# Optimization experiments

Hardware: AMD Instinct MI355X
Metric: run time of the kernel (lower is better)

## Reference

```python
import jax, jax.numpy as jnp
import numpy as np
import math

B_ = 32      # input capsule types
C_ = 32      # output capsule types
K = 3        # kernel
STRIDE = 2
H = 4
HH = H * H
ITER = 3
EPS = 1e-10
LN_2PI = math.log(2.0 * math.pi)


def setup_inputs() -> dict:
    key = jax.random.key(0)
    k1, k2, k3, k4, k5 = jax.random.split(key, 5)
    b, win = 8, 14
    poses = jax.random.normal(k1, (b, B_, win, win, HH), jnp.float32)
    activations = jax.random.uniform(k2, (b, B_, win, win), jnp.float32)
    W = jax.random.normal(k3, (B_, K, K, C_, H, H), jnp.float32)
    beta_v = jax.random.normal(k4, (1, C_, 1, 1), jnp.float32)
    beta_a = jax.random.normal(k5, (1, C_, 1), jnp.float32)
    lambda_ = jnp.float32(0.01)
    return {"poses": poses, "activations": activations, "W": W,
            "beta_v": beta_v, "beta_a": beta_a, "lambda_": lambda_}


def _extract_patches(x, w):
    r = STRIDE * jnp.arange(w)[:, None] + jnp.arange(K)  # [w, K]
    x = x[:, :, r]
    x = x[:, :, :, :, r]        # index width   -> [b,B,w_i,Kr,w_j,Kc,...]
    return x


def _em_routing(lambda_, a_, V, beta_v, beta_a):
    # a_: [b,Bkk,Cww], V: [b,Bkk,Cww,hh]
    b, Bkk, Cww, hh = V.shape
    R = jnp.full((b, Bkk, Cww), 1.0 / C_, V.dtype)
    a = None
    mu = None
    for i in range(ITER):
        Rw = (R * a_)[..., None]                      # [b,Bkk,Cww,1]
        sum_R = Rw.sum(1)                             # [b,Cww,1]
        mu = ((Rw * V).sum(1) / sum_R)[:, None]       # [b,1,Cww,hh]
        V_minus_mu_sqr = (V - mu) ** 2                # [b,Bkk,Cww,hh]
        sigma_sq = ((Rw * V_minus_mu_sqr).sum(1) / sum_R)[:, None]  # [b,1,Cww,hh]
        log_sigma = jnp.log(jnp.sqrt(sigma_sq) + EPS)
        cost = (beta_v + log_sigma.reshape(b, C_, -1, hh)) * sum_R.reshape(b, C_, -1, 1)
        a = jax.nn.sigmoid(lambda_ * (beta_a - cost.sum(-1)))
        a = a.reshape(b, Cww)
        if i != ITER - 1:
            ln_p = -V_minus_mu_sqr / (2.0 * sigma_sq) - log_sigma - 0.5 * LN_2PI
            p = jnp.exp(ln_p)
            ap = a[:, None, :] * p.sum(-1)            # [b,Bkk,Cww]
            R = jax.lax.stop_gradient(ap / (ap.sum(2, keepdims=True) + EPS) + EPS)
    return a, mu


def reference(poses, activations, W, beta_v, beta_a, lambda_):
    b = poses.shape[0]
    win = poses.shape[2]
    w = (win - K) // STRIDE + 1
    Bkk = K * K * B_
    Cww = w * w * C_

    # pose patches, ordered exactly like torch: stacked over (j outer, i inner)
    pp = _extract_patches(poses, w)                 # [b,B,w_i,Kr,w_j,Kc,hh]
    pp = pp.transpose(0, 1, 3, 5, 4, 2, 6)          # [b,B,Kr,Kc,w_j,w_i,hh]
    pp = pp.reshape(b, B_, K, K, w, w, H, H)

    # votes: W[B,Kr,Kc,C,p,q] @ pose[...,q,r]
    votes = jnp.einsum('Buvcpq,bBuvxyqr->bBuvcxypr', W, pp)
    votes = votes.reshape(b, Bkk, Cww, HH)

    # activation patches, repeated over C to match Cww=(C,w,w) flatten order
    ap = _extract_patches(activations, w)           # [b,B,w_i,Kr,w_j,Kc]
    ap = ap.transpose(0, 1, 3, 5, 4, 2).reshape(b, Bkk, w * w)
    a_ = jnp.broadcast_to(ap[:, :, None, :], (b, Bkk, C_, w * w)).reshape(b, Bkk, Cww)

    a, mu = _em_routing(lambda_, a_, votes, beta_v, beta_a)
    return mu.reshape(b, C_, w, w, HH), a.reshape(b, C_, w, w)
```

## Files before the change

### kernel.cpp

```cpp
#include <hip/hip_runtime.h>
#include <math.h>

#define NB   8
#define BC   32
#define WIN  14
#define HH   16
#define BKK  288
#define CWW  1152
#define NXY  36
#define EPSF 1e-10f
#define LOG2E 1.4426950408889634f
#define LN2   0.6931471805599453f
#define L2SQ2PI 1.3257480647361593f

__device__ __forceinline__ float ex2(float x) { return __builtin_amdgcn_exp2f(x); }
__device__ __forceinline__ float lg2(float x) { return __builtin_amdgcn_logf(x); }
__device__ __forceinline__ float rcpf(float x) { return __builtin_amdgcn_rcpf(x); }

__device__ __forceinline__ float red16(float v) {
    v += __shfl_xor(v, 1);
    v += __shfl_xor(v, 2);
    v += __shfl_xor(v, 4);
    v += __shfl_xor(v, 8);
    return v;
}

__device__ __forceinline__ float4 f4mul(float s, float4 b) {
    return make_float4(s * b.x, s * b.y, s * b.z, s * b.w);
}
__device__ __forceinline__ float4 f4fma(float s, float4 b, float4 c) {
    return make_float4(fmaf(s, b.x, c.x), fmaf(s, b.y, c.y),
                       fmaf(s, b.z, c.z), fmaf(s, b.w, c.w));
}

__global__ __launch_bounds__(256)
void wt_kernel(const float4* __restrict__ W4, float4* __restrict__ Wt4) {
    int o = blockIdx.x * 256 + threadIdx.x;
    if (o < BKK * 128) {
        int c = o & 31, p = (o >> 5) & 3, m = o >> 7;
        Wt4[o] = W4[(m * 32 + c) * 4 + p];
    }
}

__global__ __launch_bounds__(256)
void rowred_kernel(const float* __restrict__ rows_part, float* __restrict__ invRowG) {
    int i = blockIdx.x * 256 + threadIdx.x;
    if (i < NB * BKK) {
        int b = i / BKK, m = i % BKK;
        float s = EPSF;
        #pragma unroll 8
        for (int j = 0; j < 72; ++j) s += rows_part[(b * 72 + j) * BKK + m];
        invRowG[i] = 1.0f / s;
    }
}

template<int STAGE, bool FINAL>
__global__ __launch_bounds__(256)
void stats_kernel(const float* __restrict__ poses,
                  const float* __restrict__ act,
                  const float4* __restrict__ Wt4,
                  const float* __restrict__ beta_v,
                  const float* __restrict__ beta_a,
                  const float* __restrict__ lam,
                  const float* __restrict__ aws_in,
                  const float* __restrict__ psum,
                  const float* __restrict__ invRowG,
                  float* __restrict__ mu_out,
                  float* __restrict__ K2n_out,
                  float* __restrict__ C2n_out,
                  float* __restrict__ a_out)
{
    __shared__ float4 poseS4[BKK * 4];
    __shared__ float2 AE[BKK];
    __shared__ float4 red4[4 * 16 * 9];

    const int bid   = blockIdx.x;
    const int chalf = bid & 1;
    const int xy    = (bid >> 1) % NXY;
    const int b     = bid / 72;
    const int X = xy / 6, Y = xy % 6;

    const int tid = threadIdx.x;
    const int c_l = tid & 15;
    const int mch = tid >> 4;
    const int c   = chalf * 16 + c_l;
    const int n   = c * NXY + xy;

    const float4* poses4 = reinterpret_cast<const float4*>(poses);
    for (int idx = tid; idx < BKK * 4; idx += 256) {
        int m = idx >> 2, q = idx & 3;
        int B = m / 9, uv = m % 9, u = uv / 3, v = uv % 3;
        poseS4[idx] = poses4[((b * BC + B) * 196 + (2 * Y + u) * WIN + (2 * X + v)) * 4 + q];
    }
    for (int m = tid; m < BKK; m += 256) {
        int B = m / 9, uv = m % 9, u = uv / 3, v = uv % 3;
        float am = act[(b * BC + B) * 196 + (2 * Y + u) * WIN + (2 * X + v)];
        float ai, ea;
        if constexpr (STAGE == 0) { ai = am * (1.0f / 32.0f); ea = 0.0f; }
        else { ai = am * invRowG[b * BKK + m]; ea = EPSF * am; }
        AE[m] = make_float2(ai, ea);
    }

    float ap_n = 0.0f;
    const float* psum_b = nullptr;
    if constexpr (STAGE >= 1) {
        ap_n   = aws_in[(b * NXY + xy) * 32 + c];
        psum_b = psum + ((b * BKK) * NXY + xy) * 32 + c;
    }
    __syncthreads();

    const float4* WtB = Wt4 + c;

    float  sum_R = 0.0f;
    float4 sRV[4]  = {make_float4(0,0,0,0), make_float4(0,0,0,0), make_float4(0,0,0,0), make_float4(0,0,0,0)};
    float4 sRV2[4] = {make_float4(0,0,0,0), make_float4(0,0,0,0), make_float4(0,0,0,0), make_float4(0,0,0,0)};

    const int m0 = mch * 18;
    #pragma unroll 3
    for (int i = 0; i < 18; ++i) {
        int m = m0 + i;
        float4 w0 = WtB[m * 128 +  0];
        float4 w1 = WtB[m * 128 + 32];
        float4 w2 = WtB[m * 128 + 64];
        float4 w3 = WtB[m * 128 + 96];
        float4 P0 = poseS4[m * 4 + 0];
        float4 P1 = poseS4[m * 4 + 1];
        float4 P2 = poseS4[m * 4 + 2];
        float4 P3 = poseS4[m * 4 + 3];
        float4 V0 = f4fma(w0.w, P3, f4fma(w0.z, P2, f4fma(w0.y, P1, f4mul(w0.x, P0))));
        float4 V1 = f4fma(w1.w, P3, f4fma(w1.z, P2, f4fma(w1.y, P1, f4mul(w1.x, P0))));
        float4 V2 = f4fma(w2.w, P3, f4fma(w2.z, P2, f4fma(w2.y, P1, f4mul(w2.x, P0))));
        float4 V3 = f4fma(w3.w, P3, f4fma(w3.z, P2, f4fma(w3.y, P1, f4mul(w3.x, P0))));
        float Ra;
        if constexpr (STAGE == 0) {
            Ra = AE[m].x;
        } else {
            float ps = psum_b[m * (NXY * 32)];
            float2 ae = AE[m];
            Ra = fmaf(ap_n * ps, ae.x, ae.y);
        }
        sum_R += Ra;
        sRV[0] = f4fma(Ra, V0, sRV[0]);
        sRV[1] = f4fma(Ra, V1, sRV[1]);
        sRV[2] = f4fma(Ra, V2, sRV[2]);
        sRV[3] = f4fma(Ra, V3, sRV[3]);
        float4 q0 = make_float4(V0.x*V0.x, V0.y*V0.y, V0.z*V0.z, V0.w*V0.w);
        float4 q1 = make_float4(V1.x*V1.x, V1.y*V1.y, V1.z*V1.z, V1.w*V1.w);
        float4 q2 = make_float4(V2.x*V2.x, V2.y*V2.y, V2.z*V2.z, V2.w*V2.w);
        float4 q3 = make_float4(V3.x*V3.x, V3.y*V3.y, V3.z*V3.z, V3.w*V3.w);
        sRV2[0] = f4fma(Ra, q0, sRV2[0]);
        sRV2[1] = f4fma(Ra, q1, sRV2[1]);
        sRV2[2] = f4fma(Ra, q2, sRV2[2]);
        sRV2[3] = f4fma(Ra, q3, sRV2[3]);
    }

    {
        float* f1 = reinterpret_cast<float*>(sRV);
        float* f2 = reinterpret_cast<float*>(sRV2);
        #pragma unroll
        for (int k = 0; k < 16; ++k) { f1[k] += __shfl_xor(f1[k], 16); f2[k] += __shfl_xor(f2[k], 16); }
        sum_R += __shfl_xor(sum_R, 16);
        #pragma unroll
        for (int k = 0; k < 16; ++k) { f1[k] += __shfl_xor(f1[k], 32); f2[k] += __shfl_xor(f2[k], 32); }
        sum_R += __shfl_xor(sum_R, 32);
    }
    const int wgrp = tid >> 6;
    if ((tid & 48) == 0) {
        float4* dst = &red4[(wgrp * 16 + c_l) * 9];
        dst[0] = make_float4(sum_R, 0.f, 0.f, 0.f);
        dst[1] = sRV[0];  dst[2] = sRV[1];  dst[3] = sRV[2];  dst[4] = sRV[3];
        dst[5] = sRV2[0]; dst[6] = sRV2[1]; dst[7] = sRV2[2]; dst[8] = sRV2[3];
    }
    __syncthreads();

    const int h  = tid & 15;
    const int cc = tid >> 4;
    const float* red = reinterpret_cast<const float*>(red4);
    float sR = 0.f, sV = 0.f, sV2 = 0.f;
    #pragma unroll
    for (int j = 0; j < 4; ++j) {
        int off = (j * 16 + cc) * 36;
        sR  += red[off];
        sV  += red[off + 4 + h];
        sV2 += red[off + 20 + h];
    }
    float inv = 1.0f / sR;
    float mu  = sV * inv;
    float sig = fmaxf(fmaf(-mu, mu, sV2 * inv), 1e-30f);
    float l2s = lg2(sqrtf(sig) + EPSF);
    float lsum = red16(l2s) * LN2;
    int   cg   = chalf * 16 + cc;
    float cost = sR * fmaf(16.0f, beta_v[cg], lsum);
    float z    = lam[0] * (beta_a[cg] - cost);
    float av   = rcpf(1.0f + ex2(-z * LOG2E));

    int nn   = cg * NXY + xy;
    int base = (b * CWW + nn) * HH + h;
    mu_out[base] = mu;
    if constexpr (!FINAL) {
        K2n_out[base] = (-0.5f * LOG2E) / sig;
        C2n_out[base] = -(l2s + L2SQ2PI);
        if (h == 0) a_out[(b * NXY + xy) * 32 + cg] = av;
    } else {
        if (h == 0) a_out[b * CWW + nn] = av;
    }
}

__global__ __launch_bounds__(256)
void pv_kernel(const float* __restrict__ poses,
               const float4* __restrict__ Wt4,
               const float4* __restrict__ mu4,
               const float4* __restrict__ K4,
               const float4* __restrict__ C4,
               const float* __restrict__ aws,
               float* __restrict__ psum_out,
               float* __restrict__ rows_part)
{
    __shared__ float4 poseS4[BKK * 4];

    const int bid   = blockIdx.x;
    const int chalf = bid & 1;
    const int xy    = (bid >> 1) % NXY;
    const int b     = bid / 72;
    const int X = xy / 6, Y = xy % 6;

    const int tid = threadIdx.x;
    const int c_l = tid & 15;
    const int mch = tid >> 4;
    const int c   = chalf * 16 + c_l;
    const int n   = c * NXY + xy;

    const float4* poses4 = reinterpret_cast<const float4*>(poses);
    for (int idx = tid; idx < BKK * 4; idx += 256) {
        int m = idx >> 2, q = idx & 3;
        int B = m / 9, uv = m % 9, u = uv / 3, v = uv % 3;
        poseS4[idx] = poses4[((b * BC + B) * 196 + (2 * Y + u) * WIN + (2 * X + v)) * 4 + q];
    }

    float4 M[4], Kk[4], Cc[4];
    {
        int nb4 = (b * CWW + n) * 4;
        #pragma unroll
        for (int p = 0; p < 4; ++p) { M[p] = mu4[nb4 + p]; Kk[p] = K4[nb4 + p]; Cc[p] = C4[nb4 + p]; }
    }
    const float ap = aws[(b * NXY + xy) * 32 + c];
    __syncthreads();

    const float4* WtB = Wt4 + c;
    float* ps_out = psum_out + ((b * BKK) * NXY + xy) * 32 + c;
    const int rbase = bid * BKK;

    const int m0 = mch * 18;
    #pragma unroll 3
    for (int i = 0; i < 18; ++i) {
        int m = m0 + i;
        float4 w0 = WtB[m * 128 +  0];
        float4 w1 = WtB[m * 128 + 32];
        float4 w2 = WtB[m * 128 + 64];
        float4 w3 = WtB[m * 128 + 96];
        float4 P0 = poseS4[m * 4 + 0];
        float4 P1 = poseS4[m * 4 + 1];
        float4 P2 = poseS4[m * 4 + 2];
        float4 P3 = poseS4[m * 4 + 3];
        float4 V0 = f4fma(w0.w, P3, f4fma(w0.z, P2, f4fma(w0.y, P1, f4mul(w0.x, P0))));
        float4 V1 = f4fma(w1.w, P3, f4fma(w1.z, P2, f4fma(w1.y, P1, f4mul(w1.x, P0))));
        float4 V2 = f4fma(w2.w, P3, f4fma(w2.z, P2, f4fma(w2.y, P1, f4mul(w2.x, P0))));
        float4 V3 = f4fma(w3.w, P3, f4fma(w3.z, P2, f4fma(w3.y, P1, f4mul(w3.x, P0))));

        float psv = 0.0f;
        {
            float4 t, g;
            t = make_float4(V0.x-M[0].x, V0.y-M[0].y, V0.z-M[0].z, V0.w-M[0].w);
            g = make_float4(fmaf(t.x*t.x, Kk[0].x, Cc[0].x), fmaf(t.y*t.y, Kk[0].y, Cc[0].y),
                            fmaf(t.z*t.z, Kk[0].z, Cc[0].z), fmaf(t.w*t.w, Kk[0].w, Cc[0].w));
            psv += ex2(g.x) + ex2(g.y) + ex2(g.z) + ex2(g.w);
            t = make_float4(V1.x-M[1].x, V1.y-M[1].y, V1.z-M[1].z, V1.w-M[1].w);
            g = make_float4(fmaf(t.x*t.x, Kk[1].x, Cc[1].x), fmaf(t.y*t.y, Kk[1].y, Cc[1].y),
                            fmaf(t.z*t.z, Kk[1].z, Cc[1].z), fmaf(t.w*t.w, Kk[1].w, Cc[1].w));
            psv += ex2(g.x) + ex2(g.y) + ex2(g.z) + ex2(g.w);
            t = make_float4(V2.x-M[2].x, V2.y-M[2].y, V2.z-M[2].z, V2.w-M[2].w);
            g = make_float4(fmaf(t.x*t.x, Kk[2].x, Cc[2].x), fmaf(t.y*t.y, Kk[2].y, Cc[2].y),
                            fmaf(t.z*t.z, Kk[2].z, Cc[2].z), fmaf(t.w*t.w, Kk[2].w, Cc[2].w));
            psv += ex2(g.x) + ex2(g.y) + ex2(g.z) + ex2(g.w);
            t = make_float4(V3.x-M[3].x, V3.y-M[3].y, V3.z-M[3].z, V3.w-M[3].w);
            g = make_float4(fmaf(t.x*t.x, Kk[3].x, Cc[3].x), fmaf(t.y*t.y, Kk[3].y, Cc[3].y),
                            fmaf(t.z*t.z, Kk[3].z, Cc[3].z), fmaf(t.w*t.w, Kk[3].w, Cc[3].w));
            psv += ex2(g.x) + ex2(g.y) + ex2(g.z) + ex2(g.w);
        }
        ps_out[m * (NXY * 32)] = psv;

        float rv = ap * psv;
        rv += __shfl_xor(rv, 1);
        rv += __shfl_xor(rv, 2);
        rv += __shfl_xor(rv, 4);
        rv += __shfl_xor(rv, 8);
        if (c_l == 0) rows_part[rbase + m] = rv;
    }
}

extern "C" void kernel_launch(void* const* d_in, const int* in_sizes, int n_in,
                              void* d_out, int out_size, void* d_ws, size_t ws_size,
                              hipStream_t stream) {
    const float* poses  = (const float*)d_in[0];
    const float* act    = (const float*)d_in[1];
    const float* W      = (const float*)d_in[2];
    const float* beta_v = (const float*)d_in[3];
    const float* beta_a = (const float*)d_in[4];
    const float* lam    = (const float*)d_in[5];
    float* out = (float*)d_out;
    float* ws  = (float*)d_ws;

    const int SZ = NB * CWW * HH;
    float* Wt   = ws;
    float* mu   = Wt + SZ;
    float* K2n  = mu + SZ;
    float* C2n  = K2n + SZ;
    float* aws  = C2n + SZ;
    float* rows = aws + NB * CWW;
    float* invR = rows + NB * 72 * BKK;
    float* psum = invR + NB * BKK;

    const float4* Wt4 = (const float4*)Wt;

    wt_kernel<<<dim3(144), dim3(256), 0, stream>>>((const float4*)W, (float4*)Wt);

    stats_kernel<0, false><<<dim3(576), dim3(256), 0, stream>>>(
        poses, act, Wt4, beta_v, beta_a, lam, nullptr, nullptr, nullptr,
        mu, K2n, C2n, aws);
    pv_kernel<<<dim3(576), dim3(256), 0, stream>>>(
        poses, Wt4, (const float4*)mu, (const float4*)K2n, (const float4*)C2n,
        aws, psum, rows);
    rowred_kernel<<<dim3(9), dim3(256), 0, stream>>>(rows, invR);
    stats_kernel<1, false><<<dim3(576), dim3(256), 0, stream>>>(
        poses, act, Wt4, beta_v, beta_a, lam, aws, psum, invR,
        mu, K2n, C2n, aws);
    pv_kernel<<<dim3(576), dim3(256), 0, stream>>>(
        poses, Wt4, (const float4*)mu, (const float4*)K2n, (const float4*)C2n,
        aws, psum, rows);
    rowred_kernel<<<dim3(9), dim3(256), 0, stream>>>(rows, invR);
    stats_kernel<1, true><<<dim3(576), dim3(256), 0, stream>>>(
        poses, act, Wt4, beta_v, beta_a, lam, aws, psum, invR,
        out, nullptr, nullptr, out + SZ);
}
```

Before: 179.8 us.

## Fuse EM routing iterations into one persistent kernel with grid barriers

Replaces the chain of stats, pv and row-reduction kernels with a single persistent kernel. Each block keeps its pose tile, per-capsule mu, K and C terms and the p-sums in shared memory across iterations. Blocks sync through a software grid barrier built on atomics, and each block then computes the row normalisation redundantly for its batch. This removes several launches and the global round-trips of mu, K, C and psum, but it relies on all 576 blocks being co-resident (launch_bounds 256,3) and adds barrier spin cost.

```diff
diff --git a/kernel.cpp b/kernel.cpp
--- a/kernel.cpp
+++ b/kernel.cpp
@@ -8,6 +8,7 @@
 #define BKK  288
 #define CWW  1152
 #define NXY  36
+#define NBLK 576
 #define EPSF 1e-10f
 #define LOG2E 1.4426950408889634f
 #define LN2   0.6931471805599453f
@@ -33,46 +34,58 @@
                        fmaf(s, b.z, c.z), fmaf(s, b.w, c.w));
 }
 
+__device__ __forceinline__ void grid_barrier(unsigned* cnt, unsigned* gen) {
+    __threadfence();
+    __syncthreads();
+    if (threadIdx.x == 0) {
+        unsigned g = __hip_atomic_load(gen, __ATOMIC_RELAXED, __HIP_MEMORY_SCOPE_AGENT);
+        unsigned prev = __hip_atomic_fetch_add(cnt, 1u, __ATOMIC_ACQ_REL, __HIP_MEMORY_SCOPE_AGENT);
+        if (prev == NBLK - 1u) {
+            __hip_atomic_store(cnt, 0u, __ATOMIC_RELAXED, __HIP_MEMORY_SCOPE_AGENT);
+            __threadfence();
+            __hip_atomic_fetch_add(gen, 1u, __ATOMIC_RELEASE, __HIP_MEMORY_SCOPE_AGENT);
+        } else {
+            while (__hip_atomic_load(gen, __ATOMIC_RELAXED, __HIP_MEMORY_SCOPE_AGENT) == g) {
+                __builtin_amdgcn_s_sleep(2);
+            }
+        }
+    }
+    __syncthreads();
+    __threadfence();
+}
+
 __global__ __launch_bounds__(256)
-void wt_kernel(const float4* __restrict__ W4, float4* __restrict__ Wt4) {
+void wt_kernel(const float4* __restrict__ W4, float4* __restrict__ Wt4,
+               unsigned* __restrict__ bar) {
     int o = blockIdx.x * 256 + threadIdx.x;
+    if (o < 2) bar[o] = 0u;
     if (o < BKK * 128) {
         int c = o & 31, p = (o >> 5) & 3, m = o >> 7;
         Wt4[o] = W4[(m * 32 + c) * 4 + p];
     }
 }
 
-__global__ __launch_bounds__(256)
-void rowred_kernel(const float* __restrict__ rows_part, float* __restrict__ invRowG) {
-    int i = blockIdx.x * 256 + threadIdx.x;
-    if (i < NB * BKK) {
-        int b = i / BKK, m = i % BKK;
-        float s = EPSF;
-        #pragma unroll 8
-        for (int j = 0; j < 72; ++j) s += rows_part[(b * 72 + j) * BKK + m];
-        invRowG[i] = 1.0f / s;
-    }
-}
-
-template<int STAGE, bool FINAL>
-__global__ __launch_bounds__(256)
-void stats_kernel(const float* __restrict__ poses,
-                  const float* __restrict__ act,
-                  const float4* __restrict__ Wt4,
-                  const float* __restrict__ beta_v,
-                  const float* __restrict__ beta_a,
-                  const float* __restrict__ lam,
-                  const float* __restrict__ aws_in,
-                  const float* __restrict__ psum,
-                  const float* __restrict__ invRowG,
-                  float* __restrict__ mu_out,
-                  float* __restrict__ K2n_out,
-                  float* __restrict__ C2n_out,
-                  float* __restrict__ a_out)
+__global__ __launch_bounds__(256, 3)
+void fused_em(const float* __restrict__ poses,
+              const float* __restrict__ act,
+              const float4* __restrict__ Wt4,
+              const float* __restrict__ beta_v,
+              const float* __restrict__ beta_a,
+              const float* __restrict__ lam,
+              float* __restrict__ rows0,
+              float* __restrict__ rows1,
+              unsigned* __restrict__ bar,
+              float* __restrict__ mu_out,
+              float* __restrict__ a_out)
 {
     __shared__ float4 poseS4[BKK * 4];
+    __shared__ float  amL[BKK];
     __shared__ float2 AE[BKK];
-    __shared__ float4 red4[4 * 16 * 9];
+    __shared__ float  muL[16][17];
+    __shared__ float  KL[16][17];
+    __shared__ float  CL[16][17];
+    __shared__ float  aL[16];
+    __shared__ __align__(16) float uni[BKK * 17];
 
     const int bid   = blockIdx.x;
     const int chalf = bid & 1;
@@ -84,7 +97,7 @@
     const int c_l = tid & 15;
     const int mch = tid >> 4;
     const int c   = chalf * 16 + c_l;
-    const int n   = c * NXY + xy;
+    const int m0  = mch * 18;
 
     const float4* poses4 = reinterpret_cast<const float4*>(poses);
     for (int idx = tid; idx < BKK * 4; idx += 256) {
@@ -95,206 +108,182 @@
     for (int m = tid; m < BKK; m += 256) {
         int B = m / 9, uv = m % 9, u = uv / 3, v = uv % 3;
         float am = act[(b * BC + B) * 196 + (2 * Y + u) * WIN + (2 * X + v)];
-        float ai, ea;
-        if constexpr (STAGE == 0) { ai = am * (1.0f / 32.0f); ea = 0.0f; }
-        else { ai = am * invRowG[b * BKK + m]; ea = EPSF * am; }
-        AE[m] = make_float2(ai, ea);
-    }
-
-    float ap_n = 0.0f;
-    const float* psum_b = nullptr;
-    if constexpr (STAGE >= 1) {
-        ap_n   = aws_in[(b * NXY + xy) * 32 + c];
-        psum_b = psum + ((b * BKK) * NXY + xy) * 32 + c;
-    }
+        amL[m] = am;
+        AE[m] = make_float2(am * (1.0f / 32.0f), 0.0f);
+    }
+    for (int i = tid; i < BKK * 17; i += 256) uni[i] = 0.0f;
+    if (tid < 16) aL[tid] = 0.0f;
     __syncthreads();
 
-    const float4* WtB = Wt4 + c;
-
-    float  sum_R = 0.0f;
-    float4 sRV[4]  = {make_float4(0,0,0,0), make_float4(0,0,0,0), make_float4(0,0,0,0), make_float4(0,0,0,0)};
-    float4 sRV2[4] = {make_float4(0,0,0,0), make_float4(0,0,0,0), make_float4(0,0,0,0), make_float4(0,0,0,0)};
-
-    const int m0 = mch * 18;
-    #pragma unroll 3
-    for (int i = 0; i < 18; ++i) {
-        int m = m0 + i;
-        float4 w0 = WtB[m * 128 +  0];
-        float4 w1 = WtB[m * 128 + 32];
-        float4 w2 = WtB[m * 128 + 64];
-        float4 w3 = WtB[m * 128 + 96];
-        float4 P0 = poseS4[m * 4 + 0];
-        float4 P1 = poseS4[m * 4 + 1];
-        float4 P2 = poseS4[m * 4 + 2];
-        float4 P3 = poseS4[m * 4 + 3];
-        float4 V0 = f4fma(w0.w, P3, f4fma(w0.z, P2, f4fma(w0.y, P1, f4mul(w0.x, P0))));
-        float4 V1 = f4fma(w1.w, P3, f4fma(w1.z, P2, f4fma(w1.y, P1, f4mul(w1.x, P0))));
-        float4 V2 = f4fma(w2.w, P3, f4fma(w2.z, P2, f4fma(w2.y, P1, f4mul(w2.x, P0))));
-        float4 V3 = f4fma(w3.w, P3, f4fma(w3.z, P2, f4fma(w3.y, P1, f4mul(w3.x, P0))));
-        float Ra;
-        if constexpr (STAGE == 0) {
-            Ra = AE[m].x;
-        } else {
-            float ps = psum_b[m * (NXY * 32)];
+    const float4* WtB  = Wt4 + c;
+    const float   lamv = lam[0];
+    float4* red4 = reinterpret_cast<float4*>(uni);
+    unsigned* bcnt = bar;
+    unsigned* bgen = bar + 1;
+
+    for (int it = 0; it < 3; ++it) {
+        const float ap_n = aL[c_l];
+        float  sum_R = 0.0f;
+        float4 sRV[4]  = {make_float4(0,0,0,0), make_float4(0,0,0,0),
+                          make_float4(0,0,0,0), make_float4(0,0,0,0)};
+        float4 sRV2[4] = {make_float4(0,0,0,0), make_float4(0,0,0,0),
+                          make_float4(0,0,0,0), make_float4(0,0,0,0)};
+        #pragma unroll 3
+        for (int i = 0; i < 18; ++i) {
+            const int m = m0 + i;
+            float4 w0 = WtB[m * 128 +  0];
+            float4 w1 = WtB[m * 128 + 32];
+            float4 w2 = WtB[m * 128 + 64];
+            float4 w3 = WtB[m * 128 + 96];
+            float4 P0 = poseS4[m * 4 + 0];
+            float4 P1 = poseS4[m * 4 + 1];
+            float4 P2 = poseS4[m * 4 + 2];
+            float4 P3 = poseS4[m * 4 + 3];
+            float4 V0 = f4fma(w0.w, P3, f4fma(w0.z, P2, f4fma(w0.y, P1, f4mul(w0.x, P0))));
+            float4 V1 = f4fma(w1.w, P3, f4fma(w1.z, P2, f4fma(w1.y, P1, f4mul(w1.x, P0))));
+            float4 V2 = f4fma(w2.w, P3, f4fma(w2.z, P2, f4fma(w2.y, P1, f4mul(w2.x, P0))));
+            float4 V3 = f4fma(w3.w, P3, f4fma(w3.z, P2, f4fma(w3.y, P1, f4mul(w3.x, P0))));
             float2 ae = AE[m];
-            Ra = fmaf(ap_n * ps, ae.x, ae.y);
-        }
-        sum_R += Ra;
-        sRV[0] = f4fma(Ra, V0, sRV[0]);
-        sRV[1] = f4fma(Ra, V1, sRV[1]);
-        sRV[2] = f4fma(Ra, V2, sRV[2]);
-        sRV[3] = f4fma(Ra, V3, sRV[3]);
-        float4 q0 = make_float4(V0.x*V0.x, V0.y*V0.y, V0.z*V0.z, V0.w*V0.w);
-        float4 q1 = make_float4(V1.x*V1.x, V1.y*V1.y, V1.z*V1.z, V1.w*V1.w);
-        float4 q2 = make_float4(V2.x*V2.x, V2.y*V2.y, V2.z*V2.z, V2.w*V2.w);
-        float4 q3 = make_float4(V3.x*V3.x, V3.y*V3.y, V3.z*V3.z, V3.w*V3.w);
-        sRV2[0] = f4fma(Ra, q0, sRV2[0]);
-        sRV2[1] = f4fma(Ra, q1, sRV2[1]);
-        sRV2[2] = f4fma(Ra, q2, sRV2[2]);
-        sRV2[3] = f4fma(Ra, q3, sRV2[3]);
-    }
-
-    {
-        float* f1 = reinterpret_cast<float*>(sRV);
-        float* f2 = reinterpret_cast<float*>(sRV2);
+            float Ra;
+            if (it == 0) Ra = ae.x;
+            else         Ra = fmaf(ap_n * uni[m * 17 + c_l], ae.x, ae.y);
+            sum_R += Ra;
+            sRV[0] = f4fma(Ra, V0, sRV[0]);
+            sRV[1] = f4fma(Ra, V1, sRV[1]);
+            sRV[2] = f4fma(Ra, V2, sRV[2]);
+            sRV[3] = f4fma(Ra, V3, sRV[3]);
+            float4 q0 = make_float4(V0.x*V0.x, V0.y*V0.y, V0.z*V0.z, V0.w*V0.w);
+            float4 q1 = make_float4(V1.x*V1.x, V1.y*V1.y, V1.z*V1.z, V1.w*V1.w);
+            float4 q2 = make_float4(V2.x*V2.x, V2.y*V2.y, V2.z*V2.z, V2.w*V2.w);
+            float4 q3 = make_float4(V3.x*V3.x, V3.y*V3.y, V3.z*V3.z, V3.w*V3.w);
+            sRV2[0] = f4fma(Ra, q0, sRV2[0]);
+            sRV2[1] = f4fma(Ra, q1, sRV2[1]);
+            sRV2[2] = f4fma(Ra, q2, sRV2[2]);
+            sRV2[3] = f4fma(Ra, q3, sRV2[3]);
+        }
+
+        {
+            float* f1 = reinterpret_cast<float*>(sRV);
+            float* f2 = reinterpret_cast<float*>(sRV2);
+            #pragma unroll
+            for (int k = 0; k < 16; ++k) { f1[k] += __shfl_xor(f1[k], 16); f2[k] += __shfl_xor(f2[k], 16); }
+            sum_R += __shfl_xor(sum_R, 16);
+            #pragma unroll
+            for (int k = 0; k < 16; ++k) { f1[k] += __shfl_xor(f1[k], 32); f2[k] += __shfl_xor(f2[k], 32); }
+            sum_R += __shfl_xor(sum_R, 32);
+        }
+        __syncthreads();
+        if ((tid & 48) == 0) {
+            float4* dst = &red4[((tid >> 6) * 16 + c_l) * 9];
+            dst[0] = make_float4(sum_R, 0.f, 0.f, 0.f);
+            dst[1] = sRV[0];  dst[2] = sRV[1];  dst[3] = sRV[2];  dst[4] = sRV[3];
+            dst[5] = sRV2[0]; dst[6] = sRV2[1]; dst[7] = sRV2[2]; dst[8] = sRV2[3];
+        }
+        __syncthreads();
+
+        {
+            const int h  = tid & 15;
+            const int cc = tid >> 4;
+            float sR = 0.f, sV = 0.f, sV2 = 0.f;
+            #pragma unroll
+            for (int j = 0; j < 4; ++j) {
+                int off = (j * 16 + cc) * 36;
+                sR  += uni[off];
+                sV  += uni[off + 4 + h];
+                sV2 += uni[off + 20 + h];
+            }
+            float inv = 1.0f / sR;
+            float mu  = sV * inv;
+            float sig = fmaxf(fmaf(-mu, mu, sV2 * inv), 1e-30f);
+            float l2s = lg2(sqrtf(sig) + EPSF);
+            float lsum = red16(l2s) * LN2;
+            int   cgi  = chalf * 16 + cc;
+            float cost = sR * fmaf(16.0f, beta_v[cgi], lsum);
+            float z    = lamv * (beta_a[cgi] - cost);
+            float av   = rcpf(1.0f + ex2(-z * LOG2E));
+            if (it < 2) {
+                muL[cc][h] = mu;
+                KL[cc][h]  = (-0.5f * LOG2E) / sig;
+                CL[cc][h]  = -(l2s + L2SQ2PI);
+                if (h == 0) aL[cc] = av;
+            } else {
+                int nn   = cgi * NXY + xy;
+                int base = (b * CWW + nn) * HH + h;
+                mu_out[base] = mu;
+                if (h == 0) a_out[b * CWW + nn] = av;
+            }
+        }
+        if (it == 2) return;
+        __syncthreads();
+
+        float4 M[4], Kk[4], Cc[4];
         #pragma unroll
-        for (int k = 0; k < 16; ++k) { f1[k] += __shfl_xor(f1[k], 16); f2[k] += __shfl_xor(f2[k], 16); }
-        sum_R += __shfl_xor(sum_R, 16);
-        #pragma unroll
-        for (int k = 0; k < 16; ++k) { f1[k] += __shfl_xor(f1[k], 32); f2[k] += __shfl_xor(f2[k], 32); }
-        sum_R += __shfl_xor(sum_R, 32);
-    }
-    const int wgrp = tid >> 6;
-    if ((tid & 48) == 0) {
-        float4* dst = &red4[(wgrp * 16 + c_l) * 9];
-        dst[0] = make_float4(sum_R, 0.f, 0.f, 0.f);
-        dst[1] = sRV[0];  dst[2] = sRV[1];  dst[3] = sRV[2];  dst[4] = sRV[3];
-        dst[5] = sRV2[0]; dst[6] = sRV2[1]; dst[7] = sRV2[2]; dst[8] = sRV2[3];
-    }
-    __syncthreads();
-
-    const int h  = tid & 15;
-    const int cc = tid >> 4;
-    const float* red = reinterpret_cast<const float*>(red4);
-    float sR = 0.f, sV = 0.f, sV2 = 0.f;
-    #pragma unroll
-    for (int j = 0; j < 4; ++j) {
-        int off = (j * 16 + cc) * 36;
-        sR  += red[off];
-        sV  += red[off + 4 + h];
-        sV2 += red[off + 20 + h];
-    }
-    float inv = 1.0f / sR;
-    float mu  = sV * inv;
-    float sig = fmaxf(fmaf(-mu, mu, sV2 * inv), 1e-30f);
-    float l2s = lg2(sqrtf(sig) + EPSF);
-    float lsum = red16(l2s) * LN2;
-    int   cg   = chalf * 16 + cc;
-    float cost = sR * fmaf(16.0f, beta_v[cg], lsum);
-    float z    = lam[0] * (beta_a[cg] - cost);
-    float av   = rcpf(1.0f + ex2(-z * LOG2E));
-
-    int nn   = cg * NXY + xy;
-    int base = (b * CWW + nn) * HH + h;
-    mu_out[base] = mu;
-    if constexpr (!FINAL) {
-        K2n_out[base] = (-0.5f * LOG2E) / sig;
-        C2n_out[base] = -(l2s + L2SQ2PI);
-        if (h == 0) a_out[(b * NXY + xy) * 32 + cg] = av;
-    } else {
-        if (h == 0) a_out[b * CWW + nn] = av;
-    }
-}
-
-__global__ __launch_bounds__(256)
-void pv_kernel(const float* __restrict__ poses,
-               const float4* __restrict__ Wt4,
-               const float4* __restrict__ mu4,
-               const float4* __restrict__ K4,
-               const float4* __restrict__ C4,
-               const float* __restrict__ aws,
-               float* __restrict__ psum_out,
-               float* __restrict__ rows_part)
-{
-    __shared__ float4 poseS4[BKK * 4];
-
-    const int bid   = blockIdx.x;
-    const int chalf = bid & 1;
-    const int xy    = (bid >> 1) % NXY;
-    const int b     = bid / 72;
-    const int X = xy / 6, Y = xy % 6;
-
-    const int tid = threadIdx.x;
-    const int c_l = tid & 15;
-    const int mch = tid >> 4;
-    const int c   = chalf * 16 + c_l;
-    const int n   = c * NXY + xy;
-
-    const float4* poses4 = reinterpret_cast<const float4*>(poses);
-    for (int idx = tid; idx < BKK * 4; idx += 256) {
-        int m = idx >> 2, q = idx & 3;
-        int B = m / 9, uv = m % 9, u = uv / 3, v = uv % 3;
-        poseS4[idx] = poses4[((b * BC + B) * 196 + (2 * Y + u) * WIN + (2 * X + v)) * 4 + q];
-    }
-
-    float4 M[4], Kk[4], Cc[4];
-    {
-        int nb4 = (b * CWW + n) * 4;
-        #pragma unroll
-        for (int p = 0; p < 4; ++p) { M[p] = mu4[nb4 + p]; Kk[p] = K4[nb4 + p]; Cc[p] = C4[nb4 + p]; }
-    }
-    const float ap = aws[(b * NXY + xy) * 32 + c];
-    __syncthreads();
-
-    const float4* WtB = Wt4 + c;
-    float* ps_out = psum_out + ((b * BKK) * NXY + xy) * 32 + c;
-    const int rbase = bid * BKK;
-
-    const int m0 = mch * 18;
-    #pragma unroll 3
-    for (int i = 0; i < 18; ++i) {
-        int m = m0 + i;
-        float4 w0 = WtB[m * 128 +  0];
-        float4 w1 = WtB[m * 128 + 32];
-        float4 w2 = WtB[m * 128 + 64];
-        float4 w3 = WtB[m * 128 + 96];
-        float4 P0 = poseS4[m * 4 + 0];
-        float4 P1 = poseS4[m * 4 + 1];
-        float4 P2 = poseS4[m * 4 + 2];
-        float4 P3 = poseS4[m * 4 + 3];
-        float4 V0 = f4fma(w0.w, P3, f4fma(w0.z, P2, f4fma(w0.y, P1, f4mul(w0.x, P0))));
-        float4 V1 = f4fma(w1.w, P3, f4fma(w1.z, P2, f4fma(w1.y, P1, f4mul(w1.x, P0))));
-        float4 V2 = f4fma(w2.w, P3, f4fma(w2.z, P2, f4fma(w2.y, P1, f4mul(w2.x, P0))));
-        float4 V3 = f4fma(w3.w, P3, f4fma(w3.z, P2, f4fma(w3.y, P1, f4mul(w3.x, P0))));
-
-        float psv = 0.0f;
-        {
-            float4 t, g;
-            t = make_float4(V0.x-M[0].x, V0.y-M[0].y, V0.z-M[0].z, V0.w-M[0].w);
-            g = make_float4(fmaf(t.x*t.x, Kk[0].x, Cc[0].x), fmaf(t.y*t.y, Kk[0].y, Cc[0].y),
-                            fmaf(t.z*t.z, Kk[0].z, Cc[0].z), fmaf(t.w*t.w, Kk[0].w, Cc[0].w));
-            psv += ex2(g.x) + ex2(g.y) + ex2(g.z) + ex2(g.w);
-            t = make_float4(V1.x-M[1].x, V1.y-M[1].y, V1.z-M[1].z, V1.w-M[1].w);
-            g = make_float4(fmaf(t.x*t.x, Kk[1].x, Cc[1].x), fmaf(t.y*t.y, Kk[1].y, Cc[1].y),
-                            fmaf(t.z*t.z, Kk[1].z, Cc[1].z), fmaf(t.w*t.w, Kk[1].w, Cc[1].w));
-            psv += ex2(g.x) + ex2(g.y) + ex2(g.z) + ex2(g.w);
-            t = make_float4(V2.x-M[2].x, V2.y-M[2].y, V2.z-M[2].z, V2.w-M[2].w);
-            g = make_float4(fmaf(t.x*t.x, Kk[2].x, Cc[2].x), fmaf(t.y*t.y, Kk[2].y, Cc[2].y),
-                            fmaf(t.z*t.z, Kk[2].z, Cc[2].z), fmaf(t.w*t.w, Kk[2].w, Cc[2].w));
-            psv += ex2(g.x) + ex2(g.y) + ex2(g.z) + ex2(g.w);
-            t = make_float4(V3.x-M[3].x, V3.y-M[3].y, V3.z-M[3].z, V3.w-M[3].w);
-            g = make_float4(fmaf(t.x*t.x, Kk[3].x, Cc[3].x), fmaf(t.y*t.y, Kk[3].y, Cc[3].y),
-                            fmaf(t.z*t.z, Kk[3].z, Cc[3].z), fmaf(t.w*t.w, Kk[3].w, Cc[3].w));
-            psv += ex2(g.x) + ex2(g.y) + ex2(g.z) + ex2(g.w);
-        }
-        ps_out[m * (NXY * 32)] = psv;
-
-        float rv = ap * psv;
-        rv += __shfl_xor(rv, 1);
-        rv += __shfl_xor(rv, 2);
-        rv += __shfl_xor(rv, 4);
-        rv += __shfl_xor(rv, 8);
-        if (c_l == 0) rows_part[rbase + m] = rv;
+        for (int p = 0; p < 4; ++p) {
+            M[p]  = make_float4(muL[c_l][4*p+0], muL[c_l][4*p+1], muL[c_l][4*p+2], muL[c_l][4*p+3]);
+            Kk[p] = make_float4(KL[c_l][4*p+0],  KL[c_l][4*p+1],  KL[c_l][4*p+2],  KL[c_l][4*p+3]);
+            Cc[p] = make_float4(CL[c_l][4*p+0],  CL[c_l][4*p+1],  CL[c_l][4*p+2],  CL[c_l][4*p+3]);
+        }
+        const float ap = aL[c_l];
+        float* rowsW = (it == 0 ? rows0 : rows1) + bid * BKK;
+
+        #pragma unroll 3
+        for (int i = 0; i < 18; ++i) {
+            const int m = m0 + i;
+            float4 w0 = WtB[m * 128 +  0];
+            float4 w1 = WtB[m * 128 + 32];
+            float4 w2 = WtB[m * 128 + 64];
+            float4 w3 = WtB[m * 128 + 96];
+            float4 P0 = poseS4[m * 4 + 0];
+            float4 P1 = poseS4[m * 4 + 1];
+            float4 P2 = poseS4[m * 4 + 2];
+            float4 P3 = poseS4[m * 4 + 3];
+            float4 V0 = f4fma(w0.w, P3, f4fma(w0.z, P2, f4fma(w0.y, P1, f4mul(w0.x, P0))));
+            float4 V1 = f4fma(w1.w, P3, f4fma(w1.z, P2, f4fma(w1.y, P1, f4mul(w1.x, P0))));
+            float4 V2 = f4fma(w2.w, P3, f4fma(w2.z, P2, f4fma(w2.y, P1, f4mul(w2.x, P0))));
+            float4 V3 = f4fma(w3.w, P3, f4fma(w3.z, P2, f4fma(w3.y, P1, f4mul(w3.x, P0))));
+
+            float psv = 0.0f;
+            {
+                float4 t, g;
+                t = make_float4(V0.x-M[0].x, V0.y-M[0].y, V0.z-M[0].z, V0.w-M[0].w);
+                g = make_float4(fmaf(t.x*t.x, Kk[0].x, Cc[0].x), fmaf(t.y*t.y, Kk[0].y, Cc[0].y),
+                                fmaf(t.z*t.z, Kk[0].z, Cc[0].z), fmaf(t.w*t.w, Kk[0].w, Cc[0].w));
+                psv += ex2(g.x) + ex2(g.y) + ex2(g.z) + ex2(g.w);
+                t = make_float4(V1.x-M[1].x, V1.y-M[1].y, V1.z-M[1].z, V1.w-M[1].w);
+                g = make_float4(fmaf(t.x*t.x, Kk[1].x, Cc[1].x), fmaf(t.y*t.y, Kk[1].y, Cc[1].y),
+                                fmaf(t.z*t.z, Kk[1].z, Cc[1].z), fmaf(t.w*t.w, Kk[1].w, Cc[1].w));
+                psv += ex2(g.x) + ex2(g.y) + ex2(g.z) + ex2(g.w);
+                t = make_float4(V2.x-M[2].x, V2.y-M[2].y, V2.z-M[2].z, V2.w-M[2].w);
+                g = make_float4(fmaf(t.x*t.x, Kk[2].x, Cc[2].x), fmaf(t.y*t.y, Kk[2].y, Cc[2].y),
+                                fmaf(t.z*t.z, Kk[2].z, Cc[2].z), fmaf(t.w*t.w, Kk[2].w, Cc[2].w));
+                psv += ex2(g.x) + ex2(g.y) + ex2(g.z) + ex2(g.w);
+                t = make_float4(V3.x-M[3].x, V3.y-M[3].y, V3.z-M[3].z, V3.w-M[3].w);
+                g = make_float4(fmaf(t.x*t.x, Kk[3].x, Cc[3].x), fmaf(t.y*t.y, Kk[3].y, Cc[3].y),
+                                fmaf(t.z*t.z, Kk[3].z, Cc[3].z), fmaf(t.w*t.w, Kk[3].w, Cc[3].w));
+                psv += ex2(g.x) + ex2(g.y) + ex2(g.z) + ex2(g.w);
+            }
+            uni[m * 17 + c_l] = psv;
+
+            float rv = ap * psv;
+            rv += __shfl_xor(rv, 1);
+            rv += __shfl_xor(rv, 2);
+            rv += __shfl_xor(rv, 4);
+            rv += __shfl_xor(rv, 8);
+            if (c_l == 0) rowsW[m] = rv;
+        }
+
+        grid_barrier(bcnt, bgen);
+
+        const float* rowsR = (it == 0 ? rows0 : rows1) + b * 72 * BKK;
+        for (int m = tid; m < BKK; m += 256) {
+            float s = EPSF;
+            #pragma unroll 8
+            for (int j = 0; j < 72; ++j) s += rowsR[j * BKK + m];
+            float invr = 1.0f / s;
+            float am = amL[m];
+            AE[m] = make_float2(am * invr, EPSF * am);
+        }
+        __syncthreads();
     }
 }
 
@@ -311,34 +300,15 @@
     float* ws  = (float*)d_ws;
 
     const int SZ = NB * CWW * HH;
-    float* Wt   = ws;
-    float* mu   = Wt + SZ;
-    float* K2n  = mu + SZ;
-    float* C2n  = K2n + SZ;
-    float* aws  = C2n + SZ;
-    float* rows = aws + NB * CWW;
-    float* invR = rows + NB * 72 * BKK;
-    float* psum = invR + NB * BKK;
+    float* Wt    = ws;
+    float* rows0 = Wt + BKK * 512;
+    float* rows1 = rows0 + NB * 72 * BKK;
+    unsigned* bar = (unsigned*)(rows1 + NB * 72 * BKK);
+
+    wt_kernel<<<dim3(144), dim3(256), 0, stream>>>((const float4*)W, (float4*)Wt, bar);
 
     const float4* Wt4 = (const float4*)Wt;
-
-    wt_kernel<<<dim3(144), dim3(256), 0, stream>>>((const float4*)W, (float4*)Wt);
-
-    stats_kernel<0, false><<<dim3(576), dim3(256), 0, stream>>>(
-        poses, act, Wt4, beta_v, beta_a, lam, nullptr, nullptr, nullptr,
-        mu, K2n, C2n, aws);
-    pv_kernel<<<dim3(576), dim3(256), 0, stream>>>(
-        poses, Wt4, (const float4*)mu, (const float4*)K2n, (const float4*)C2n,
-        aws, psum, rows);
-    rowred_kernel<<<dim3(9), dim3(256), 0, stream>>>(rows, invR);
-    stats_kernel<1, false><<<dim3(576), dim3(256), 0, stream>>>(
-        poses, act, Wt4, beta_v, beta_a, lam, aws, psum, invR,
-        mu, K2n, C2n, aws);
-    pv_kernel<<<dim3(576), dim3(256), 0, stream>>>(
-        poses, Wt4, (const float4*)mu, (const float4*)K2n, (const float4*)C2n,
-        aws, psum, rows);
-    rowred_kernel<<<dim3(9), dim3(256), 0, stream>>>(rows, invR);
-    stats_kernel<1, true><<<dim3(576), dim3(256), 0, stream>>>(
-        poses, act, Wt4, beta_v, beta_a, lam, aws, psum, invR,
-        out, nullptr, nullptr, out + SZ);
-}
+    fused_em<<<dim3(NBLK), dim3(256), 0, stream>>>(
+        poses, act, Wt4, beta_v, beta_a, lam,
+        rows0, rows1, bar, out, out + SZ);
+}
```

Result: slower. 438.9 us (+144.1%).
